# Kernel tuning notes

Hardware: AMD Instinct MI355X
Metric: run time of the kernel (lower is better)

The kernel has to match this reference:

```python
import jax, jax.numpy as jnp
import numpy as np

B, C, L = 8, 256, 4096
OC = C // 2  # out_channels default
EPS = 1e-5


def setup_inputs() -> dict:
    key = jax.random.key(0)
    ks = jax.random.split(key, 12)
    s_in = 1.0 / np.sqrt(C)   # conv1d default init scale (kaiming-uniform-ish)
    s_oc = 1.0 / np.sqrt(OC)
    return {
        "x": jax.random.normal(ks[0], (B, C, L), dtype=jnp.float32),
        "g_w": jax.random.uniform(ks[1], (OC, C), jnp.float32, -s_in, s_in),
        "g_b": jax.random.uniform(ks[2], (OC,), jnp.float32, -s_in, s_in),
        # theta/phi weights: nn.init.normal_(w, 0.02) -> mean 0.02, std 1
        "theta_w": 0.02 + jax.random.normal(ks[3], (OC, C), dtype=jnp.float32),
        "theta_b": jax.random.uniform(ks[4], (OC,), jnp.float32, -s_in, s_in),
        "phi_w": 0.02 + jax.random.normal(ks[5], (OC, C), dtype=jnp.float32),
        "phi_b": jax.random.uniform(ks[6], (OC,), jnp.float32, -s_in, s_in),
        "W_w": jax.random.uniform(ks[7], (C, OC), jnp.float32, -s_oc, s_oc),
        "W_b": jax.random.uniform(ks[8], (C,), jnp.float32, -s_oc, s_oc),
        # BN affine: init to zero in the original; use small random for a meaningful test
        "gamma": 0.1 * jax.random.normal(ks[9], (C,), dtype=jnp.float32),
        "beta": 0.1 * jax.random.normal(ks[10], (C,), dtype=jnp.float32),
    }


def reference(x, g_w, g_b, theta_w, theta_b, phi_w, phi_b, W_w, W_b, gamma, beta):
    # x: (b, c, l). 1x1 conv == per-position linear map over channels.
    g_x = jnp.einsum('oc,bcl->bol', g_w, x) + g_b[None, :, None]        # (b, oc, l)
    theta_x = jnp.einsum('oc,bcl->bol', theta_w, x) + theta_b[None, :, None]
    phi_x = jnp.einsum('oc,bcl->bol', phi_w, x) + phi_b[None, :, None]
    # f = theta^T phi : (b, l, l) quadratic score matrix (no softmax)
    f = jnp.einsum('bok,bom->bkm', theta_x, phi_x)
    N = f.shape[-1]
    # y = (f @ g^T) / N, returned in (b, oc, l) layout
    y = jnp.einsum('bkm,bom->bok', f, g_x) / N
    W_y = jnp.einsum('co,bol->bcl', W_w, y) + W_b[None, :, None]        # (b, c, l)
    # BatchNorm1d (training mode: batch statistics over (b, l), biased var)
    mean = jnp.mean(W_y, axis=(0, 2), keepdims=True)
    var = jnp.mean((W_y - mean) ** 2, axis=(0, 2), keepdims=True)
    W_y = (W_y - mean) * jax.lax.rsqrt(var + EPS)
    W_y = gamma[None, :, None] * W_y + beta[None, :, None]
    return W_y + x  # residual
```

## Files before the change

kernel.cpp:

```cpp
#include <hip/hip_runtime.h>
#include <hip/hip_bf16.h>

#define B_ 8
#define C_ 256
#define OC_ 128
#define L_ 4096
#define EPS_ 1e-5f
#define SPLITK 8

typedef unsigned short u16;
typedef __attribute__((ext_vector_type(4))) unsigned short u16x4;
typedef __attribute__((ext_vector_type(4))) float f32x4;
typedef __attribute__((ext_vector_type(8))) short bf16x8;

__device__ inline u16 f2bf(float f) {
  union { __hip_bfloat16 h; u16 u; } v;
  v.h = __float2bfloat16(f);
  return v.u;
}
__device__ inline float bf2f(u16 u) {
  union { float f; unsigned u; } v;
  v.u = ((unsigned)u) << 16;
  return v.f;
}

__device__ inline void gload_lds16(const void* g, void* lds) {
  __builtin_amdgcn_global_load_lds(
      (const __attribute__((address_space(1))) unsigned int*)g,
      (__attribute__((address_space(3))) unsigned int*)lds, 16, 0, 0);
}

__global__ __launch_bounds__(256) void k_cvt(const float* __restrict__ x,
                                             u16* __restrict__ Xb,
                                             u16* __restrict__ XbT,
                                             float* __restrict__ spartial) {
  __shared__ u16 T[64][73];
  __shared__ float P[64][17];
  const int b = blockIdx.z, c0 = blockIdx.y * 64, l0 = blockIdx.x * 64;
  const int tid = threadIdx.x;
#pragma unroll
  for (int it = 0; it < 4; ++it) {
    int idx = it * 256 + tid;
    int row = idx >> 4;
    int col = (idx & 15) << 2;
    size_t gi = ((size_t)(b * C_ + c0 + row)) * L_ + l0 + col;
    float4 v = *(const float4*)(x + gi);
    u16 u0 = f2bf(v.x), u1 = f2bf(v.y), u2 = f2bf(v.z), u3 = f2bf(v.w);
    u16x4 u = {u0, u1, u2, u3};
    *(u16x4*)(Xb + gi) = u;
    T[row][col] = u0; T[row][col + 1] = u1; T[row][col + 2] = u2; T[row][col + 3] = u3;
    P[row][idx & 15] = v.x + v.y + v.z + v.w;
  }
  __syncthreads();
  if (tid < 64) {
    float acc = 0.f;
#pragma unroll
    for (int j = 0; j < 16; j++) acc += P[tid][j];
    spartial[(size_t)blockIdx.x * (B_ * C_) + b * C_ + c0 + tid] = acc;
  }
#pragma unroll
  for (int it = 0; it < 4; ++it) {
    int idx = it * 256 + tid;
    int lrow = idx >> 4;
    int ccol = (idx & 15) << 2;
    u16x4 u = {T[ccol][lrow], T[ccol + 1][lrow], T[ccol + 2][lrow], T[ccol + 3][lrow]};
    *(u16x4*)(XbT + ((size_t)b * L_ + l0 + lrow) * C_ + c0 + ccol) = u;
  }
}

__global__ __launch_bounds__(256) void k_xxt(const u16* __restrict__ Xb,
                                             float* __restrict__ Spart) {
  const int b = blockIdx.z, split = blockIdx.y;
  const int ti = blockIdx.x >> 2, tj = blockIdx.x & 3;
  __shared__ u16 lds[2][2][64 * 64];
  const int tid = threadIdx.x, lane = tid & 63;
  const int wid = tid >> 6, wr = wid >> 1, wc = wid & 1;
  const u16* Arows = Xb + ((size_t)b * C_ + ti * 64) * L_;
  const u16* Brows = Xb + ((size_t)b * C_ + tj * 64) * L_;
  const int k0 = split * (L_ / SPLITK);
  f32x4 acc[2][2] = {};

  auto STAGE = [&](int buf, int kt) {
#pragma unroll
    for (int ch = 0; ch < 2; ch++) {
      int d = ch * 4096 + tid * 16;
      int row = d >> 7;
      int kb = (d & 127) ^ ((row & 7) << 4);
      gload_lds16(Arows + (size_t)row * L_ + k0 + kt + (kb >> 1), (char*)lds[buf][0] + d);
      gload_lds16(Brows + (size_t)row * L_ + k0 + kt + (kb >> 1), (char*)lds[buf][1] + d);
    }
  };

  STAGE(0, 0);
  asm volatile("s_waitcnt vmcnt(0)" ::: "memory");
  __syncthreads();
  int cur = 0;
  for (int kt = 0; kt < L_ / SPLITK; kt += 64) {
    if (kt + 64 < L_ / SPLITK) STAGE(cur ^ 1, kt + 64);
#pragma unroll
    for (int kk = 0; kk < 2; kk++) {
      bf16x8 af[2], bfr[2];
#pragma unroll
      for (int m = 0; m < 2; m++) {
        int row = wr * 32 + m * 16 + (lane & 15);
        int kb = ((kk << 6) + ((lane >> 4) << 4)) ^ ((row & 7) << 4);
        af[m] = *(const bf16x8*)((const char*)lds[cur][0] + row * 128 + kb);
      }
#pragma unroll
      for (int n = 0; n < 2; n++) {
        int row = wc * 32 + n * 16 + (lane & 15);
        int kb = ((kk << 6) + ((lane >> 4) << 4)) ^ ((row & 7) << 4);
        bfr[n] = *(const bf16x8*)((const char*)lds[cur][1] + row * 128 + kb);
      }
#pragma unroll
      for (int m = 0; m < 2; m++)
#pragma unroll
        for (int n = 0; n < 2; n++)
          acc[m][n] = __builtin_amdgcn_mfma_f32_16x16x32_bf16(af[m], bfr[n], acc[m][n], 0, 0, 0);
    }
    asm volatile("s_waitcnt vmcnt(0)" ::: "memory");
    __syncthreads();
    cur ^= 1;
  }
  float* Sp = Spart + ((size_t)split * B_ + b) * C_ * C_;
#pragma unroll
  for (int m = 0; m < 2; m++)
#pragma unroll
    for (int n = 0; n < 2; n++) {
      int r0 = ti * 64 + wr * 32 + m * 16 + ((lane >> 4) << 2);
      int c0 = tj * 64 + wc * 32 + n * 16 + (lane & 15);
#pragma unroll
      for (int r = 0; r < 4; r++)
        Sp[(size_t)(r0 + r) * C_ + c0] = acc[m][n][r];
    }
}

__global__ __launch_bounds__(256) void k_sreduce(const float* __restrict__ Spart,
                                                 const float* __restrict__ spartial,
                                                 const float* __restrict__ g_w,
                                                 float* __restrict__ S,
                                                 u16* __restrict__ Sb,
                                                 float* __restrict__ s,
                                                 float* __restrict__ gwT) {
  const int bid = blockIdx.x, tid = threadIdx.x;
  if (bid < (B_ * C_ * C_) / 256) {
    size_t idx = (size_t)bid * 256 + tid;
    float acc = 0.f;
    for (int sp = 0; sp < SPLITK; sp++) acc += Spart[(size_t)sp * B_ * C_ * C_ + idx];
    S[idx] = acc;
    Sb[idx] = f2bf(acc);
  } else if (bid < (B_ * C_ * C_) / 256 + (B_ * C_) / 256) {
    int idx2 = (bid - (B_ * C_ * C_) / 256) * 256 + tid;
    float acc = 0.f;
#pragma unroll 8
    for (int i = 0; i < 64; i++) acc += spartial[(size_t)i * (B_ * C_) + idx2];
    s[idx2] = acc;
  } else {
    int t = bid - ((B_ * C_ * C_) / 256 + (B_ * C_) / 256);
    int o = t * 8 + (tid & 7);
    int cbase = (tid >> 3) * 8;
#pragma unroll
    for (int k = 0; k < 8; k++) {
      int c = cbase + k;
      gwT[c * OC_ + o] = g_w[o * C_ + c];
    }
  }
}

__global__ __launch_bounds__(256) void k_mid1(const float* __restrict__ S,
                                              const float* __restrict__ s,
                                              const float* __restrict__ phi_w,
                                              const float* __restrict__ phi_b,
                                              const float* __restrict__ gwT,
                                              const float* __restrict__ g_b,
                                              float* __restrict__ MT) {
  const int b = blockIdx.x >> 5, ot = blockIdx.x & 31;
  const int tid = threadIdx.x;
  __shared__ float pw[4][257], t2[4][257], sl[256], ps_s[4], pb_s[4], redw[4][4];
  sl[tid] = s[b * C_ + tid];
#pragma unroll
  for (int r = 0; r < 4; r++) pw[r][tid] = phi_w[(ot * 4 + r) * C_ + tid];
  if (tid < 4) pb_s[tid] = phi_b[ot * 4 + tid];
  __syncthreads();
  float acc4[4] = {};
  const float* Sbr = S + (size_t)b * C_ * C_;
#pragma unroll 4
  for (int cp = 0; cp < C_; cp++) {
    float sv = Sbr[(size_t)cp * C_ + tid];
#pragma unroll
    for (int r = 0; r < 4; r++) acc4[r] += pw[r][cp] * sv;
  }
  const int lane = tid & 63, w = tid >> 6;
#pragma unroll
  for (int r = 0; r < 4; r++) {
    float v = pw[r][tid] * sl[tid];
#pragma unroll
    for (int off = 1; off < 64; off <<= 1) v += __shfl_xor(v, off, 64);
    if (lane == 0) redw[w][r] = v;
  }
#pragma unroll
  for (int r = 0; r < 4; r++) t2[r][tid] = acc4[r] + pb_s[r] * sl[tid];
  __syncthreads();
  if (tid < 4) ps_s[tid] = redw[0][tid] + redw[1][tid] + redw[2][tid] + redw[3][tid];
  __syncthreads();
  const int o = tid & 127, half = tid >> 7;
  float m0 = 0.f, m1 = 0.f;
#pragma unroll 4
  for (int c = 0; c < C_; c++) {
    float gv = gwT[c * OC_ + o];
    m0 += t2[half * 2][c] * gv;
    m1 += t2[half * 2 + 1][c] * gv;
  }
  float gb = g_b[o];
  int r0 = half * 2;
  MT[((size_t)b * OC_ + o) * OC_ + ot * 4 + r0]     = m0 + (ps_s[r0] + (float)L_ * pb_s[r0]) * gb;
  MT[((size_t)b * OC_ + o) * OC_ + ot * 4 + r0 + 1] = m1 + (ps_s[r0 + 1] + (float)L_ * pb_s[r0 + 1]) * gb;
}

__global__ __launch_bounds__(256) void k_mid2(const float* __restrict__ MT,
                                              const float* __restrict__ W_w,
                                              const float* __restrict__ theta_w,
                                              const float* __restrict__ theta_b,
                                              const float* __restrict__ W_b,
                                              const float* __restrict__ s,
                                              u16* __restrict__ Qb,
                                              float* __restrict__ qv,
                                              float* __restrict__ qs_g,
                                              float* __restrict__ sum1) {
  const int b = blockIdx.x >> 6, ct = blockIdx.x & 63;
  const int c0 = ct * 4;
  const int tid = threadIdx.x;
  __shared__ float ww[4][OC_], u_s[4][OC_ + 2], s_l[C_], q_s[4], redq[4][4];
  s_l[tid] = s[b * C_ + tid];
#pragma unroll
  for (int i = tid; i < 4 * OC_; i += 256)
    ww[i >> 7][i & 127] = W_w[(c0 + (i >> 7)) * OC_ + (i & 127)];
  __syncthreads();
  const int op = tid & 127, rh = tid >> 7;
  float ua0 = 0.f, ua1 = 0.f;
  const float* MTb = MT + (size_t)b * OC_ * OC_;
#pragma unroll 4
  for (int o = 0; o < OC_; o++) {
    float mv = MTb[(size_t)o * OC_ + op];
    ua0 += ww[rh * 2][o] * mv;
    ua1 += ww[rh * 2 + 1][o] * mv;
  }
  u_s[rh * 2][op] = ua0 * (1.f / (float)L_);
  u_s[rh * 2 + 1][op] = ua1 * (1.f / (float)L_);
  __syncthreads();
  {
    const int r = tid >> 6, lane = tid & 63;
    float v = u_s[r][lane] * theta_b[lane] + u_s[r][lane + 64] * theta_b[lane + 64];
#pragma unroll
    for (int off = 1; off < 64; off <<= 1) v += __shfl_xor(v, off, 64);
    if (lane == 0) {
      float qval = v + W_b[c0 + r];
      q_s[r] = qval;
      qv[b * C_ + c0 + r] = qval;
    }
  }
  float qa[4] = {};
#pragma unroll 2
  for (int o = 0; o < OC_; o++) {
    float tv = theta_w[(size_t)o * C_ + tid];
#pragma unroll
    for (int r = 0; r < 4; r++) qa[r] += u_s[r][o] * tv;
  }
#pragma unroll
  for (int r = 0; r < 4; r++)
    Qb[((size_t)b * C_ + c0 + r) * C_ + tid] = f2bf(qa[r]);
  const int lane = tid & 63, w = tid >> 6;
#pragma unroll
  for (int r = 0; r < 4; r++) {
    float v = qa[r] * s_l[tid];
#pragma unroll
    for (int off = 1; off < 64; off <<= 1) v += __shfl_xor(v, off, 64);
    if (lane == 0) redq[w][r] = v;
  }
  __syncthreads();
  if (tid < 4) {
    float qs = redq[0][tid] + redq[1][tid] + redq[2][tid] + redq[3][tid];
    qs_g[b * C_ + c0 + tid] = qs;
    sum1[b * C_ + c0 + tid] = qs + (float)L_ * q_s[tid];
  }
}

__global__ __launch_bounds__(256) void k_ystat(const u16* __restrict__ Qb,
                                               const u16* __restrict__ Sb,
                                               float* __restrict__ e2part) {
  const int b = blockIdx.z;
  const int chs = blockIdx.y >> 1, ct = blockIdx.y & 1;
  const int ks = blockIdx.x;
  __shared__ u16 lds[2 * 128 * 64];
  __shared__ float e2s[128][2];
  const int tid = threadIdx.x, lane = tid & 63;
  const int wid = tid >> 6, wr = wid >> 1, wc = wid & 1;
  const u16* Abase = Qb + ((size_t)b * C_ + ct * 128) * C_;
  const u16* Bbase = Sb + ((size_t)b * C_ + chs * 128) * C_;
  const int k0 = ks * 64;
  f32x4 acc[4][4] = {};
#pragma unroll
  for (int ch = 0; ch < 4; ch++) {
    int d = ch * 4096 + tid * 16;
    int row = d >> 7;
    int kb = (d & 127) ^ ((row & 7) << 4);
    gload_lds16(Abase + (size_t)row * C_ + k0 + (kb >> 1), (char*)lds + d);
    gload_lds16(Bbase + (size_t)row * C_ + k0 + (kb >> 1), (char*)lds + 16384 + d);
  }
  asm volatile("s_waitcnt vmcnt(0)" ::: "memory");
  __syncthreads();
#pragma unroll
  for (int kk = 0; kk < 2; kk++) {
    bf16x8 af[4], bfr[4];
#pragma unroll
    for (int m = 0; m < 4; m++) {
      int row = wr * 64 + m * 16 + (lane & 15);
      int kb = ((kk << 6) + ((lane >> 4) << 4)) ^ ((row & 7) << 4);
      af[m] = *(const bf16x8*)((const char*)lds + row * 128 + kb);
    }
#pragma unroll
    for (int n = 0; n < 4; n++) {
      int row = wc * 64 + n * 16 + (lane & 15);
      int kb = ((kk << 6) + ((lane >> 4) << 4)) ^ ((row & 7) << 4);
      bfr[n] = *(const bf16x8*)((const char*)lds + 16384 + row * 128 + kb);
    }
#pragma unroll
    for (int m = 0; m < 4; m++)
#pragma unroll
      for (int n = 0; n < 4; n++)
        acc[m][n] = __builtin_amdgcn_mfma_f32_16x16x32_bf16(af[m], bfr[n], acc[m][n], 0, 0, 0);
  }
  float e2a[4][4];
#pragma unroll
  for (int m = 0; m < 4; m++)
#pragma unroll
    for (int r = 0; r < 4; r++) e2a[m][r] = 0.f;
#pragma unroll
  for (int m = 0; m < 4; m++)
#pragma unroll
    for (int n = 0; n < 4; n++) {
      int ch = chs * 128 + wc * 64 + n * 16 + (lane & 15);
#pragma unroll
      for (int r = 0; r < 4; r++) {
        int c_loc = wr * 64 + m * 16 + ((lane >> 4) << 2) + r;
        float q2 = bf2f(Qb[((size_t)b * C_ + ct * 128 + c_loc) * C_ + ch]);
        e2a[m][r] += acc[m][n][r] * q2;
      }
    }
#pragma unroll
  for (int m = 0; m < 4; m++)
#pragma unroll
    for (int r = 0; r < 4; r++) {
      float v = e2a[m][r];
      v += __shfl_xor(v, 1, 64);
      v += __shfl_xor(v, 2, 64);
      v += __shfl_xor(v, 4, 64);
      v += __shfl_xor(v, 8, 64);
      if ((lane & 15) == 0) {
        int c_loc = wr * 64 + m * 16 + ((lane >> 4) << 2) + r;
        e2s[c_loc][wc] = v;
      }
    }
  __syncthreads();
  if (tid < 128)
    e2part[(((size_t)chs * 4 + ks) * B_ + b) * C_ + ct * 128 + tid] =
        e2s[tid][0] + e2s[tid][1];
}

__global__ __launch_bounds__(256) void k_fin(const float* __restrict__ sum1,
                                             const float* __restrict__ e2part,
                                             const float* __restrict__ qv,
                                             const float* __restrict__ qs_g,
                                             const float* __restrict__ gamma,
                                             const float* __restrict__ beta,
                                             float* __restrict__ gsc_g,
                                             float* __restrict__ qp_g) {
  const int b = blockIdx.x, c = threadIdx.x;
  float m = 0.f, e = 0.f;
#pragma unroll
  for (int bb = 0; bb < B_; bb++) {
    m += sum1[bb * C_ + c];
    float e2 = 0.f;
#pragma unroll
    for (int sl = 0; sl < 8; sl++) e2 += e2part[((size_t)sl * B_ + bb) * C_ + c];
    float qq = qv[bb * C_ + c], qs = qs_g[bb * C_ + c];
    e += e2 + 2.f * qq * qs + (float)L_ * qq * qq;
  }
  const float inv_n = 1.f / (float)(B_ * L_);
  m *= inv_n;
  e *= inv_n;
  float var = e - m * m;
  float g = gamma[c] * rsqrtf(var + EPS_);
  if (b == 0) gsc_g[c] = g;
  qp_g[b * C_ + c] = g * (qv[b * C_ + c] - m) + beta[c];
}

__global__ __launch_bounds__(256) void k_out(const u16* __restrict__ Qb,
                                             const float* __restrict__ gsc_g,
                                             const float* __restrict__ qp_g,
                                             const u16* __restrict__ XbT,
                                             const u16* __restrict__ Xb,
                                             float* __restrict__ out) {
  const int b = blockIdx.z, ct = blockIdx.y, lt = blockIdx.x;
  __shared__ u16 lds[2][2 * 128 * 64];
  __shared__ float gsc_s[128], qp_s[128];
  const int tid = threadIdx.x, lane = tid & 63;
  const int wid = tid >> 6, wr = wid >> 1, wc = wid & 1;
  if (tid < 128) {
    gsc_s[tid] = gsc_g[ct * 128 + tid];
    qp_s[tid] = qp_g[b * C_ + ct * 128 + tid];
  }
  const u16* Abase = Qb + ((size_t)b * C_ + ct * 128) * C_;
  const u16* Bbase = XbT + ((size_t)b * L_ + lt * 128) * C_;
  f32x4 acc[4][4] = {};
  auto STAGE = [&](int buf, int k0) {
#pragma unroll
    for (int ch = 0; ch < 4; ch++) {
      int d = ch * 4096 + tid * 16;
      int row = d >> 7;
      int kb = (d & 127) ^ ((row & 7) << 4);
      gload_lds16(Abase + (size_t)row * C_ + k0 + (kb >> 1), (char*)lds[buf] + d);
      gload_lds16(Bbase + (size_t)row * C_ + k0 + (kb >> 1), (char*)lds[buf] + 16384 + d);
    }
  };
  STAGE(0, 0);
  asm volatile("s_waitcnt vmcnt(0)" ::: "memory");
  __syncthreads();
  int cur = 0;
  for (int k0 = 0; k0 < C_; k0 += 64) {
    if (k0 + 64 < C_) STAGE(cur ^ 1, k0 + 64);
#pragma unroll
    for (int kk = 0; kk < 2; kk++) {
      bf16x8 af[4], bfr[4];
#pragma unroll
      for (int m = 0; m < 4; m++) {
        int row = wr * 64 + m * 16 + (lane & 15);
        int kb = ((kk << 6) + ((lane >> 4) << 4)) ^ ((row & 7) << 4);
        af[m] = *(const bf16x8*)((const char*)lds[cur] + row * 128 + kb);
      }
#pragma unroll
      for (int n = 0; n < 4; n++) {
        int row = wc * 64 + n * 16 + (lane & 15);
        int kb = ((kk << 6) + ((lane >> 4) << 4)) ^ ((row & 7) << 4);
        bfr[n] = *(const bf16x8*)((const char*)lds[cur] + 16384 + row * 128 + kb);
      }
#pragma unroll
      for (int m = 0; m < 4; m++)
#pragma unroll
        for (int n = 0; n < 4; n++)
          acc[m][n] = __builtin_amdgcn_mfma_f32_16x16x32_bf16(af[m], bfr[n], acc[m][n], 0, 0, 0);
    }
    asm volatile("s_waitcnt vmcnt(0)" ::: "memory");
    __syncthreads();
    cur ^= 1;
  }
#pragma unroll
  for (int m = 0; m < 4; m++)
#pragma unroll
    for (int n = 0; n < 4; n++) {
      int cl = wr * 64 + m * 16 + ((lane >> 4) << 2);
      int c = ct * 128 + cl;
      int l = lt * 128 + wc * 64 + n * 16 + (lane & 15);
#pragma unroll
      for (int r = 0; r < 4; r++) {
        size_t gi = ((size_t)b * C_ + c + r) * L_ + l;
        out[gi] = gsc_s[cl + r] * acc[m][n][r] + bf2f(Xb[gi]) + qp_s[cl + r];
      }
    }
}

extern "C" void kernel_launch(void* const* d_in, const int* in_sizes, int n_in,
                              void* d_out, int out_size, void* d_ws, size_t ws_size,
                              hipStream_t stream) {
  const float* x       = (const float*)d_in[0];
  const float* g_w     = (const float*)d_in[1];
  const float* g_b     = (const float*)d_in[2];
  const float* theta_w = (const float*)d_in[3];
  const float* theta_b = (const float*)d_in[4];
  const float* phi_w   = (const float*)d_in[5];
  const float* phi_b   = (const float*)d_in[6];
  const float* W_w     = (const float*)d_in[7];
  const float* W_b     = (const float*)d_in[8];
  const float* gamma   = (const float*)d_in[9];
  const float* beta    = (const float*)d_in[10];
  float* out = (float*)d_out;

  float* ws = (float*)d_ws;
  size_t off = 0;
  float* Spart    = ws + off; off += (size_t)SPLITK * B_ * C_ * C_;
  float* S        = ws + off; off += (size_t)B_ * C_ * C_;
  float* spartial = ws + off; off += (size_t)B_ * C_ * 64;
  float* s_       = ws + off; off += B_ * C_;
  float* gwT      = ws + off; off += C_ * OC_;
  float* MT       = ws + off; off += (size_t)B_ * OC_ * OC_;
  float* qv       = ws + off; off += B_ * C_;
  float* qs_g     = ws + off; off += B_ * C_;
  float* sum1     = ws + off; off += B_ * C_;
  float* e2part   = ws + off; off += 8 * B_ * C_;
  float* gsc_g    = ws + off; off += C_;
  float* qp_g     = ws + off; off += B_ * C_;
  u16* Sb  = (u16*)(ws + off); off += (size_t)B_ * C_ * C_ / 2;
  u16* Qb  = (u16*)(ws + off); off += (size_t)B_ * C_ * C_ / 2;
  u16* Xb  = (u16*)(ws + off); off += (size_t)B_ * C_ * L_ / 2;
  u16* XbT = (u16*)(ws + off); off += (size_t)B_ * C_ * L_ / 2;

  k_cvt<<<dim3(L_ / 64, C_ / 64, B_), 256, 0, stream>>>(x, Xb, XbT, spartial);
  k_xxt<<<dim3(16, SPLITK, B_), 256, 0, stream>>>(Xb, Spart);
  k_sreduce<<<(B_ * C_ * C_) / 256 + (B_ * C_) / 256 + 16, 256, 0, stream>>>(
      Spart, spartial, g_w, S, Sb, s_, gwT);
  k_mid1<<<B_ * 32, 256, 0, stream>>>(S, s_, phi_w, phi_b, gwT, g_b, MT);
  k_mid2<<<B_ * 64, 256, 0, stream>>>(MT, W_w, theta_w, theta_b, W_b, s_,
                                      Qb, qv, qs_g, sum1);
  k_ystat<<<dim3(4, 4, B_), 256, 0, stream>>>(Qb, Sb, e2part);
  k_fin<<<B_, 256, 0, stream>>>(sum1, e2part, qv, qs_g, gamma, beta, gsc_g, qp_g);
  k_out<<<dim3(L_ / 128, C_ / 128, B_), 256, 0, stream>>>(
      Qb, gsc_g, qp_g, XbT, Xb, out);
}
```

Baseline: 126.7 us.

## Precompose weight products, fuse mid kernels into MFMA Q generator, drop residual reload

Batch-independent weight products (W_w·g_w, theta_w^T·phi_w and the bias terms) are now computed in extra blocks of the conversion kernel. The per-batch reduction and the two mid kernels are replaced by a single MFMA-based kernel that reduces the split-K partials on the fly and builds Q. BatchNorm finalisation moves into the output kernel. The residual is folded into the GEMM by adding an identity to gsc·Q, so Xb is no longer re-read. SPLITK is halved, and the kernel count drops from eight to five, at the cost of a small 32-block Q stage and extra bf16 rounding of the residual path.

```diff
diff --git a/kernel.cpp b/kernel.cpp
--- a/kernel.cpp
+++ b/kernel.cpp
@@ -6,10 +6,12 @@
 #define OC_ 128
 #define L_ 4096
 #define EPS_ 1e-5f
-#define SPLITK 8
+#define SPLITK 4
+#define INV_L (1.0f / 4096.0f)
 
 typedef unsigned short u16;
 typedef __attribute__((ext_vector_type(4))) unsigned short u16x4;
+typedef __attribute__((ext_vector_type(8))) unsigned short u16x8;
 typedef __attribute__((ext_vector_type(4))) float f32x4;
 typedef __attribute__((ext_vector_type(8))) short bf16x8;
 
@@ -30,41 +32,114 @@
       (__attribute__((address_space(3))) unsigned int*)lds, 16, 0, 0);
 }
 
-__global__ __launch_bounds__(256) void k_cvt(const float* __restrict__ x,
-                                             u16* __restrict__ Xb,
-                                             u16* __restrict__ XbT,
-                                             float* __restrict__ spartial) {
+__global__ __launch_bounds__(256) void k_cvt(
+    const float* __restrict__ x, u16* __restrict__ Xb, u16* __restrict__ XbT,
+    float* __restrict__ spartial,
+    const float* __restrict__ W_w, const float* __restrict__ g_w,
+    const float* __restrict__ g_b, const float* __restrict__ theta_w,
+    const float* __restrict__ theta_b, const float* __restrict__ phi_w,
+    const float* __restrict__ phi_b,
+    u16* __restrict__ P1b, u16* __restrict__ P1Tb, u16* __restrict__ P2T,
+    float* __restrict__ w1, float* __restrict__ rho, float* __restrict__ p2b,
+    float* __restrict__ tbbg) {
+  const int bid = blockIdx.x, tid = threadIdx.x;
   __shared__ u16 T[64][73];
   __shared__ float P[64][17];
-  const int b = blockIdx.z, c0 = blockIdx.y * 64, l0 = blockIdx.x * 64;
-  const int tid = threadIdx.x;
-#pragma unroll
-  for (int it = 0; it < 4; ++it) {
-    int idx = it * 256 + tid;
-    int row = idx >> 4;
-    int col = (idx & 15) << 2;
-    size_t gi = ((size_t)(b * C_ + c0 + row)) * L_ + l0 + col;
-    float4 v = *(const float4*)(x + gi);
-    u16 u0 = f2bf(v.x), u1 = f2bf(v.y), u2 = f2bf(v.z), u3 = f2bf(v.w);
-    u16x4 u = {u0, u1, u2, u3};
-    *(u16x4*)(Xb + gi) = u;
-    T[row][col] = u0; T[row][col + 1] = u1; T[row][col + 2] = u2; T[row][col + 3] = u3;
-    P[row][idx & 15] = v.x + v.y + v.z + v.w;
-  }
-  __syncthreads();
-  if (tid < 64) {
-    float acc = 0.f;
-#pragma unroll
-    for (int j = 0; j < 16; j++) acc += P[tid][j];
-    spartial[(size_t)blockIdx.x * (B_ * C_) + b * C_ + c0 + tid] = acc;
-  }
-#pragma unroll
-  for (int it = 0; it < 4; ++it) {
-    int idx = it * 256 + tid;
-    int lrow = idx >> 4;
-    int ccol = (idx & 15) << 2;
-    u16x4 u = {T[ccol][lrow], T[ccol + 1][lrow], T[ccol + 2][lrow], T[ccol + 3][lrow]};
-    *(u16x4*)(XbT + ((size_t)b * L_ + l0 + lrow) * C_ + c0 + ccol) = u;
+  __shared__ float ww[32][OC_ + 1];
+  __shared__ float gbs[OC_];
+  __shared__ float tw[OC_][33];
+  __shared__ float pbs[OC_], tbs[OC_];
+  if (bid < 2048) {
+    const int b = bid >> 8, ct = (bid >> 6) & 3, lt = bid & 63;
+    const int c0 = ct * 64, l0 = lt * 64;
+#pragma unroll
+    for (int it = 0; it < 4; ++it) {
+      int idx = it * 256 + tid;
+      int row = idx >> 4;
+      int col = (idx & 15) << 2;
+      size_t gi = ((size_t)(b * C_ + c0 + row)) * L_ + l0 + col;
+      float4 v = *(const float4*)(x + gi);
+      u16 u0 = f2bf(v.x), u1_ = f2bf(v.y), u2 = f2bf(v.z), u3 = f2bf(v.w);
+      u16x4 u = {u0, u1_, u2, u3};
+      *(u16x4*)(Xb + gi) = u;
+      T[row][col] = u0; T[row][col + 1] = u1_; T[row][col + 2] = u2; T[row][col + 3] = u3;
+      P[row][idx & 15] = v.x + v.y + v.z + v.w;
+    }
+    __syncthreads();
+    if (tid < 64) {
+      float acc = 0.f;
+#pragma unroll
+      for (int j = 0; j < 16; j++) acc += P[tid][j];
+      spartial[(size_t)lt * (B_ * C_) + b * C_ + c0 + tid] = acc;
+    }
+#pragma unroll
+    for (int it = 0; it < 4; ++it) {
+      int idx = it * 256 + tid;
+      int lrow = idx >> 4;
+      int ccol = (idx & 15) << 2;
+      u16x4 u = {T[ccol][lrow], T[ccol + 1][lrow], T[ccol + 2][lrow], T[ccol + 3][lrow]};
+      *(u16x4*)(XbT + ((size_t)b * L_ + l0 + lrow) * C_ + c0 + ccol) = u;
+    }
+  } else if (bid < 2056) {
+    const int cbase = (bid - 2048) * 32;
+    for (int i = tid; i < 32 * OC_; i += 256)
+      ww[i >> 7][i & 127] = W_w[(size_t)(cbase + (i >> 7)) * OC_ + (i & 127)];
+    if (tid < OC_) gbs[tid] = g_b[tid];
+    __syncthreads();
+    float acc[32] = {};
+    for (int o = 0; o < OC_; o++) {
+      float gv = g_w[(size_t)o * C_ + tid];
+#pragma unroll
+      for (int r = 0; r < 32; r++) acc[r] += ww[r][o] * gv;
+    }
+    u16 tr[32];
+#pragma unroll
+    for (int r = 0; r < 32; r++) {
+      u16 h = f2bf(acc[r]);
+      P1b[(size_t)(cbase + r) * C_ + tid] = h;
+      tr[r] = h;
+    }
+#pragma unroll
+    for (int k = 0; k < 4; k++) {
+      u16x8 v;
+#pragma unroll
+      for (int j = 0; j < 8; j++) v[j] = tr[k * 8 + j];
+      *(u16x8*)(P1Tb + (size_t)tid * C_ + cbase + k * 8) = v;
+    }
+    if (tid < 32) {
+      float a = 0.f;
+      for (int o = 0; o < OC_; o++) a += ww[tid][o] * gbs[o];
+      w1[cbase + tid] = a;
+    }
+  } else {
+    const int c2base = (bid - 2056) * 32;
+    for (int i = tid; i < OC_ * 32; i += 256) {
+      int op = i >> 5, r = i & 31;
+      tw[op][r] = theta_w[(size_t)op * C_ + c2base + r];
+    }
+    if (tid < OC_) { pbs[tid] = phi_b[tid]; tbs[tid] = theta_b[tid]; }
+    __syncthreads();
+    float acc[32] = {};
+    float ap2b = 0.f;
+    for (int op = 0; op < OC_; op++) {
+      float pv = phi_w[(size_t)op * C_ + tid];
+#pragma unroll
+      for (int r = 0; r < 32; r++) acc[r] += tw[op][r] * pv;
+      ap2b += tbs[op] * pv;
+    }
+#pragma unroll
+    for (int r = 0; r < 32; r++) P2T[(size_t)(c2base + r) * C_ + tid] = f2bf(acc[r]);
+    if (bid == 2056) p2b[tid] = ap2b;
+    if (tid < 32) {
+      float a = 0.f;
+      for (int op = 0; op < OC_; op++) a += pbs[op] * tw[op][tid];
+      rho[c2base + tid] = a;
+    }
+    if (bid == 2056 && tid == 0) {
+      float a = 0.f;
+      for (int op = 0; op < OC_; op++) a += pbs[op] * tbs[op];
+      tbbg[0] = a;
+    }
   }
 }
 
@@ -135,158 +210,197 @@
     }
 }
 
-__global__ __launch_bounds__(256) void k_sreduce(const float* __restrict__ Spart,
-                                                 const float* __restrict__ spartial,
-                                                 const float* __restrict__ g_w,
-                                                 float* __restrict__ S,
-                                                 u16* __restrict__ Sb,
-                                                 float* __restrict__ s,
-                                                 float* __restrict__ gwT) {
-  const int bid = blockIdx.x, tid = threadIdx.x;
-  if (bid < (B_ * C_ * C_) / 256) {
-    size_t idx = (size_t)bid * 256 + tid;
-    float acc = 0.f;
-    for (int sp = 0; sp < SPLITK; sp++) acc += Spart[(size_t)sp * B_ * C_ * C_ + idx];
-    S[idx] = acc;
-    Sb[idx] = f2bf(acc);
-  } else if (bid < (B_ * C_ * C_) / 256 + (B_ * C_) / 256) {
-    int idx2 = (bid - (B_ * C_ * C_) / 256) * 256 + tid;
-    float acc = 0.f;
-#pragma unroll 8
-    for (int i = 0; i < 64; i++) acc += spartial[(size_t)i * (B_ * C_) + idx2];
-    s[idx2] = acc;
-  } else {
-    int t = bid - ((B_ * C_ * C_) / 256 + (B_ * C_) / 256);
-    int o = t * 8 + (tid & 7);
-    int cbase = (tid >> 3) * 8;
-#pragma unroll
-    for (int k = 0; k < 8; k++) {
-      int c = cbase + k;
-      gwT[c * OC_ + o] = g_w[o * C_ + c];
-    }
-  }
-}
-
-__global__ __launch_bounds__(256) void k_mid1(const float* __restrict__ S,
-                                              const float* __restrict__ s,
-                                              const float* __restrict__ phi_w,
-                                              const float* __restrict__ phi_b,
-                                              const float* __restrict__ gwT,
-                                              const float* __restrict__ g_b,
-                                              float* __restrict__ MT) {
-  const int b = blockIdx.x >> 5, ot = blockIdx.x & 31;
-  const int tid = threadIdx.x;
-  __shared__ float pw[4][257], t2[4][257], sl[256], ps_s[4], pb_s[4], redw[4][4];
-  sl[tid] = s[b * C_ + tid];
-#pragma unroll
-  for (int r = 0; r < 4; r++) pw[r][tid] = phi_w[(ot * 4 + r) * C_ + tid];
-  if (tid < 4) pb_s[tid] = phi_b[ot * 4 + tid];
+__global__ __launch_bounds__(256) void k_qgen(
+    const float* __restrict__ Spart, const float* __restrict__ spartial,
+    const u16* __restrict__ P1b, const u16* __restrict__ P1Tb,
+    const u16* __restrict__ P2T,
+    const float* __restrict__ w1g, const float* __restrict__ rho,
+    const float* __restrict__ p2b, const float* __restrict__ tbbg,
+    const float* __restrict__ W_b,
+    u16* __restrict__ Qb, float* __restrict__ qv, float* __restrict__ qspart) {
+  const int js = blockIdx.x, b = blockIdx.y;
+  const int tid = threadIdx.x, lane = tid & 63, wid = tid >> 6;
+  __shared__ u16 Abuf[256 * 64];
+  __shared__ u16 Bbuf[64 * 64];
+  __shared__ u16 Tt[64][264];
+  __shared__ float s_l[C_], u1_l[C_], z_l[C_], p2b_l[C_], w1_l[C_];
+  __shared__ float v1_l[64], red[4];
+  {
+    float a = 0.f;
+    for (int lt = 0; lt < 64; lt++) a += spartial[(size_t)lt * (B_ * C_) + b * C_ + tid];
+    s_l[tid] = a;
+    p2b_l[tid] = p2b[tid];
+    w1_l[tid] = w1g[tid];
+  }
+  float part = s_l[tid] * p2b_l[tid];
+#pragma unroll
+  for (int off = 1; off < 64; off <<= 1) part += __shfl_xor(part, off, 64);
+  if (lane == 0) red[wid] = part;
   __syncthreads();
-  float acc4[4] = {};
-  const float* Sbr = S + (size_t)b * C_ * C_;
+  const float sp2b = red[0] + red[1] + red[2] + red[3];
+  f32x4 acc[4][4] = {};
+  for (int kt = 0; kt < C_; kt += 64) {
+    __syncthreads();
+    {
+      const int jr = (tid & 15) * 4;
+      const int rb = tid >> 4;
 #pragma unroll 4
-  for (int cp = 0; cp < C_; cp++) {
-    float sv = Sbr[(size_t)cp * C_ + tid];
-#pragma unroll
-    for (int r = 0; r < 4; r++) acc4[r] += pw[r][cp] * sv;
-  }
-  const int lane = tid & 63, w = tid >> 6;
-#pragma unroll
-  for (int r = 0; r < 4; r++) {
-    float v = pw[r][tid] * sl[tid];
-#pragma unroll
-    for (int off = 1; off < 64; off <<= 1) v += __shfl_xor(v, off, 64);
-    if (lane == 0) redw[w][r] = v;
-  }
-#pragma unroll
-  for (int r = 0; r < 4; r++) t2[r][tid] = acc4[r] + pb_s[r] * sl[tid];
+      for (int pass = 0; pass < 16; pass++) {
+        int row = pass * 16 + rb;
+        float4 a0 = {0.f, 0.f, 0.f, 0.f};
+#pragma unroll
+        for (int sp = 0; sp < SPLITK; sp++) {
+          float4 v = *(const float4*)(Spart + ((size_t)sp * B_ + b) * (C_ * C_) +
+                                      (size_t)row * C_ + kt + jr);
+          a0.x += v.x; a0.y += v.y; a0.z += v.z; a0.w += v.w;
+        }
+        u16x4 h = {f2bf(a0.x), f2bf(a0.y), f2bf(a0.z), f2bf(a0.w)};
+        int byte = (jr * 2) ^ ((row & 7) << 4);
+        *(u16x4*)((char*)Abuf + row * 128 + byte) = h;
+      }
+#pragma unroll
+      for (int ch = 0; ch < 2; ch++) {
+        int d = ch * 4096 + tid * 16;
+        int row = d >> 7;
+        int kb = (d & 127) ^ ((row & 7) << 4);
+        gload_lds16(P2T + (size_t)(js * 64 + row) * C_ + kt + (kb >> 1), (char*)Bbuf + d);
+      }
+    }
+    asm volatile("s_waitcnt vmcnt(0)" ::: "memory");
+    __syncthreads();
+#pragma unroll
+    for (int kk = 0; kk < 2; kk++) {
+      bf16x8 af[4], bfr[4];
+#pragma unroll
+      for (int m = 0; m < 4; m++) {
+        int row = wid * 64 + m * 16 + (lane & 15);
+        int kb = ((kk << 6) + ((lane >> 4) << 4)) ^ ((row & 7) << 4);
+        af[m] = *(const bf16x8*)((const char*)Abuf + row * 128 + kb);
+      }
+#pragma unroll
+      for (int n = 0; n < 4; n++) {
+        int row = n * 16 + (lane & 15);
+        int kb = ((kk << 6) + ((lane >> 4) << 4)) ^ ((row & 7) << 4);
+        bfr[n] = *(const bf16x8*)((const char*)Bbuf + row * 128 + kb);
+      }
+#pragma unroll
+      for (int m = 0; m < 4; m++)
+#pragma unroll
+        for (int n = 0; n < 4; n++)
+          acc[m][n] = __builtin_amdgcn_mfma_f32_16x16x32_bf16(af[m], bfr[n], acc[m][n], 0, 0, 0);
+    }
+  }
+#pragma unroll
+  for (int m = 0; m < 4; m++)
+#pragma unroll
+    for (int n = 0; n < 4; n++) {
+      int j = n * 16 + (lane & 15);
+      int t0 = wid * 64 + m * 16 + ((lane >> 4) << 2);
+      u16x4 h = {f2bf(acc[m][n][0]), f2bf(acc[m][n][1]), f2bf(acc[m][n][2]), f2bf(acc[m][n][3])};
+      *(u16x4*)((char*)&Tt[0][0] + j * 528 + t0 * 2) = h;
+    }
+  {
+    float a = 0.f;
+    for (int cp = 0; cp < C_; cp++) a += bf2f(P1Tb[(size_t)cp * C_ + tid]) * s_l[cp];
+    u1_l[tid] = a;
+  }
+  if (tid < 64) {
+    float a = 0.f;
+    const u16x8* pr = (const u16x8*)(P2T + (size_t)(js * 64 + tid) * C_);
+    for (int i = 0; i < 32; i++) {
+      u16x8 v = pr[i];
+#pragma unroll
+      for (int k = 0; k < 8; k++) a += bf2f(v[k]) * s_l[i * 8 + k];
+    }
+    v1_l[tid] = a;
+  }
+  if (js == 0) {
+    float a = 0.f;
+    for (int sp = 0; sp < SPLITK; sp++)
+      for (int cp = 0; cp < C_; cp++)
+        a += Spart[((size_t)sp * B_ + b) * (C_ * C_) + (size_t)cp * C_ + tid] * p2b_l[cp];
+    z_l[tid] = a;
+  }
   __syncthreads();
-  if (tid < 4) ps_s[tid] = redw[0][tid] + redw[1][tid] + redw[2][tid] + redw[3][tid];
-  __syncthreads();
-  const int o = tid & 127, half = tid >> 7;
-  float m0 = 0.f, m1 = 0.f;
-#pragma unroll 4
-  for (int c = 0; c < C_; c++) {
-    float gv = gwT[c * OC_ + o];
-    m0 += t2[half * 2][c] * gv;
-    m1 += t2[half * 2 + 1][c] * gv;
-  }
-  float gb = g_b[o];
-  int r0 = half * 2;
-  MT[((size_t)b * OC_ + o) * OC_ + ot * 4 + r0]     = m0 + (ps_s[r0] + (float)L_ * pb_s[r0]) * gb;
-  MT[((size_t)b * OC_ + o) * OC_ + ot * 4 + r0 + 1] = m1 + (ps_s[r0 + 1] + (float)L_ * pb_s[r0 + 1]) * gb;
-}
-
-__global__ __launch_bounds__(256) void k_mid2(const float* __restrict__ MT,
-                                              const float* __restrict__ W_w,
-                                              const float* __restrict__ theta_w,
-                                              const float* __restrict__ theta_b,
-                                              const float* __restrict__ W_b,
-                                              const float* __restrict__ s,
-                                              u16* __restrict__ Qb,
-                                              float* __restrict__ qv,
-                                              float* __restrict__ qs_g,
-                                              float* __restrict__ sum1) {
-  const int b = blockIdx.x >> 6, ct = blockIdx.x & 63;
-  const int c0 = ct * 4;
-  const int tid = threadIdx.x;
-  __shared__ float ww[4][OC_], u_s[4][OC_ + 2], s_l[C_], q_s[4], redq[4][4];
-  s_l[tid] = s[b * C_ + tid];
-#pragma unroll
-  for (int i = tid; i < 4 * OC_; i += 256)
-    ww[i >> 7][i & 127] = W_w[(c0 + (i >> 7)) * OC_ + (i & 127)];
-  __syncthreads();
-  const int op = tid & 127, rh = tid >> 7;
-  float ua0 = 0.f, ua1 = 0.f;
-  const float* MTb = MT + (size_t)b * OC_ * OC_;
-#pragma unroll 4
-  for (int o = 0; o < OC_; o++) {
-    float mv = MTb[(size_t)o * OC_ + op];
-    ua0 += ww[rh * 2][o] * mv;
-    ua1 += ww[rh * 2 + 1][o] * mv;
-  }
-  u_s[rh * 2][op] = ua0 * (1.f / (float)L_);
-  u_s[rh * 2 + 1][op] = ua1 * (1.f / (float)L_);
-  __syncthreads();
-  {
-    const int r = tid >> 6, lane = tid & 63;
-    float v = u_s[r][lane] * theta_b[lane] + u_s[r][lane + 64] * theta_b[lane + 64];
-#pragma unroll
-    for (int off = 1; off < 64; off <<= 1) v += __shfl_xor(v, off, 64);
-    if (lane == 0) {
-      float qval = v + W_b[c0 + r];
-      q_s[r] = qval;
-      qv[b * C_ + c0 + r] = qval;
-    }
-  }
-  float qa[4] = {};
-#pragma unroll 2
-  for (int o = 0; o < OC_; o++) {
-    float tv = theta_w[(size_t)o * C_ + tid];
-#pragma unroll
-    for (int r = 0; r < 4; r++) qa[r] += u_s[r][o] * tv;
-  }
-#pragma unroll
-  for (int r = 0; r < 4; r++)
-    Qb[((size_t)b * C_ + c0 + r) * C_ + tid] = f2bf(qa[r]);
-  const int lane = tid & 63, w = tid >> 6;
-#pragma unroll
-  for (int r = 0; r < 4; r++) {
-    float v = qa[r] * s_l[tid];
-#pragma unroll
-    for (int off = 1; off < 64; off <<= 1) v += __shfl_xor(v, off, 64);
-    if (lane == 0) redq[w][r] = v;
-  }
-  __syncthreads();
-  if (tid < 4) {
-    float qs = redq[0][tid] + redq[1][tid] + redq[2][tid] + redq[3][tid];
-    qs_g[b * C_ + c0 + tid] = qs;
-    sum1[b * C_ + c0 + tid] = qs + (float)L_ * q_s[tid];
+  if (js == 0) {
+    float qq = 0.f;
+    for (int cp = 0; cp < C_; cp++) qq += bf2f(P1Tb[(size_t)cp * C_ + tid]) * z_l[cp];
+    float tbb = tbbg[0];
+    float w1c = w1_l[tid];
+    qv[b * C_ + tid] = INV_L * (qq + w1c * sp2b + u1_l[tid] * tbb) + w1c * tbb + W_b[tid];
+  }
+  f32x4 acc2[4][4] = {};
+  for (int kt = 0; kt < C_; kt += 64) {
+    __syncthreads();
+#pragma unroll
+    for (int ch = 0; ch < 8; ch++) {
+      int d = ch * 4096 + tid * 16;
+      int row = d >> 7;
+      int kb = (d & 127) ^ ((row & 7) << 4);
+      gload_lds16(P1b + (size_t)row * C_ + kt + (kb >> 1), (char*)Abuf + d);
+    }
+    asm volatile("s_waitcnt vmcnt(0)" ::: "memory");
+    __syncthreads();
+#pragma unroll
+    for (int kk = 0; kk < 2; kk++) {
+      bf16x8 af[4], bfr[4];
+#pragma unroll
+      for (int m = 0; m < 4; m++) {
+        int row = wid * 64 + m * 16 + (lane & 15);
+        int kb = ((kk << 6) + ((lane >> 4) << 4)) ^ ((row & 7) << 4);
+        af[m] = *(const bf16x8*)((const char*)Abuf + row * 128 + kb);
+      }
+#pragma unroll
+      for (int n = 0; n < 4; n++) {
+        int j = n * 16 + (lane & 15);
+        int ke = kt + kk * 32 + ((lane >> 4) << 3);
+        bfr[n] = *(const bf16x8*)((const char*)&Tt[0][0] + j * 528 + ke * 2);
+      }
+#pragma unroll
+      for (int m = 0; m < 4; m++)
+#pragma unroll
+        for (int n = 0; n < 4; n++)
+          acc2[m][n] = __builtin_amdgcn_mfma_f32_16x16x32_bf16(af[m], bfr[n], acc2[m][n], 0, 0, 0);
+    }
+  }
+  float rho_j[4], v1_j[4];
+#pragma unroll
+  for (int n = 0; n < 4; n++) {
+    rho_j[n] = rho[js * 64 + n * 16 + (lane & 15)];
+    v1_j[n] = v1_l[n * 16 + (lane & 15)];
+  }
+#pragma unroll
+  for (int m = 0; m < 4; m++) {
+    int c0 = wid * 64 + m * 16 + ((lane >> 4) << 2);
+    float qsp_acc[4] = {};
+#pragma unroll
+    for (int n = 0; n < 4; n++) {
+      int jg = js * 64 + n * 16 + (lane & 15);
+      float sj = s_l[jg];
+#pragma unroll
+      for (int r = 0; r < 4; r++) {
+        int c = c0 + r;
+        float q = INV_L * acc2[m][n][r] + w1_l[c] * (INV_L * v1_j[n] + rho_j[n]) +
+                  INV_L * u1_l[c] * rho_j[n];
+        Qb[((size_t)b * C_ + c) * C_ + jg] = f2bf(q);
+        qsp_acc[r] += q * sj;
+      }
+    }
+#pragma unroll
+    for (int r = 0; r < 4; r++) {
+      float v = qsp_acc[r];
+      v += __shfl_xor(v, 1, 64);
+      v += __shfl_xor(v, 2, 64);
+      v += __shfl_xor(v, 4, 64);
+      v += __shfl_xor(v, 8, 64);
+      if ((lane & 15) == 0)
+        qspart[((size_t)js * B_ + b) * C_ + c0 + r] = v;
+    }
   }
 }
 
 __global__ __launch_bounds__(256) void k_ystat(const u16* __restrict__ Qb,
-                                               const u16* __restrict__ Sb,
+                                               const float* __restrict__ Spart,
                                                float* __restrict__ e2part) {
   const int b = blockIdx.z;
   const int chs = blockIdx.y >> 1, ct = blockIdx.y & 1;
@@ -296,7 +410,6 @@
   const int tid = threadIdx.x, lane = tid & 63;
   const int wid = tid >> 6, wr = wid >> 1, wc = wid & 1;
   const u16* Abase = Qb + ((size_t)b * C_ + ct * 128) * C_;
-  const u16* Bbase = Sb + ((size_t)b * C_ + chs * 128) * C_;
   const int k0 = ks * 64;
   f32x4 acc[4][4] = {};
 #pragma unroll
@@ -305,7 +418,24 @@
     int row = d >> 7;
     int kb = (d & 127) ^ ((row & 7) << 4);
     gload_lds16(Abase + (size_t)row * C_ + k0 + (kb >> 1), (char*)lds + d);
-    gload_lds16(Bbase + (size_t)row * C_ + k0 + (kb >> 1), (char*)lds + 16384 + d);
+  }
+  {
+    const int jr = (tid & 15) * 4;
+    const int rb = tid >> 4;
+#pragma unroll 4
+    for (int pass = 0; pass < 8; pass++) {
+      int row = pass * 16 + rb;
+      float4 a0 = {0.f, 0.f, 0.f, 0.f};
+#pragma unroll
+      for (int sp = 0; sp < SPLITK; sp++) {
+        float4 v = *(const float4*)(Spart + ((size_t)sp * B_ + b) * (C_ * C_) +
+                                    (size_t)(chs * 128 + row) * C_ + k0 + jr);
+        a0.x += v.x; a0.y += v.y; a0.z += v.z; a0.w += v.w;
+      }
+      u16x4 h = {f2bf(a0.x), f2bf(a0.y), f2bf(a0.z), f2bf(a0.w)};
+      int byte = (jr * 2) ^ ((row & 7) << 4);
+      *(u16x4*)((char*)lds + 16384 + row * 128 + byte) = h;
+    }
   }
   asm volatile("s_waitcnt vmcnt(0)" ::: "memory");
   __syncthreads();
@@ -367,68 +497,94 @@
         e2s[tid][0] + e2s[tid][1];
 }
 
-__global__ __launch_bounds__(256) void k_fin(const float* __restrict__ sum1,
+__global__ __launch_bounds__(256) void k_out(const u16* __restrict__ Qb,
+                                             const float* __restrict__ qv,
+                                             const float* __restrict__ qspart,
                                              const float* __restrict__ e2part,
-                                             const float* __restrict__ qv,
-                                             const float* __restrict__ qs_g,
                                              const float* __restrict__ gamma,
                                              const float* __restrict__ beta,
-                                             float* __restrict__ gsc_g,
-                                             float* __restrict__ qp_g) {
-  const int b = blockIdx.x, c = threadIdx.x;
-  float m = 0.f, e = 0.f;
-#pragma unroll
-  for (int bb = 0; bb < B_; bb++) {
-    m += sum1[bb * C_ + c];
-    float e2 = 0.f;
-#pragma unroll
-    for (int sl = 0; sl < 8; sl++) e2 += e2part[((size_t)sl * B_ + bb) * C_ + c];
-    float qq = qv[bb * C_ + c], qs = qs_g[bb * C_ + c];
-    e += e2 + 2.f * qq * qs + (float)L_ * qq * qq;
-  }
-  const float inv_n = 1.f / (float)(B_ * L_);
-  m *= inv_n;
-  e *= inv_n;
-  float var = e - m * m;
-  float g = gamma[c] * rsqrtf(var + EPS_);
-  if (b == 0) gsc_g[c] = g;
-  qp_g[b * C_ + c] = g * (qv[b * C_ + c] - m) + beta[c];
-}
-
-__global__ __launch_bounds__(256) void k_out(const u16* __restrict__ Qb,
-                                             const float* __restrict__ gsc_g,
-                                             const float* __restrict__ qp_g,
                                              const u16* __restrict__ XbT,
-                                             const u16* __restrict__ Xb,
                                              float* __restrict__ out) {
   const int b = blockIdx.z, ct = blockIdx.y, lt = blockIdx.x;
-  __shared__ u16 lds[2][2 * 128 * 64];
+  __shared__ u16 Albs[2][128 * 64];
+  __shared__ u16 Blbs[2][128 * 64];
   __shared__ float gsc_s[128], qp_s[128];
   const int tid = threadIdx.x, lane = tid & 63;
   const int wid = tid >> 6, wr = wid >> 1, wc = wid & 1;
   if (tid < 128) {
-    gsc_s[tid] = gsc_g[ct * 128 + tid];
-    qp_s[tid] = qp_g[b * C_ + ct * 128 + tid];
-  }
-  const u16* Abase = Qb + ((size_t)b * C_ + ct * 128) * C_;
+    int c = ct * 128 + tid;
+    float m_ = 0.f, e_ = 0.f;
+#pragma unroll
+    for (int bb = 0; bb < B_; bb++) {
+      float qsv = 0.f;
+#pragma unroll
+      for (int jss = 0; jss < 4; jss++) qsv += qspart[((size_t)jss * B_ + bb) * C_ + c];
+      float qvv = qv[bb * C_ + c];
+      m_ += qsv + (float)L_ * qvv;
+      float e2 = 0.f;
+#pragma unroll
+      for (int sl = 0; sl < 8; sl++) e2 += e2part[((size_t)sl * B_ + bb) * C_ + c];
+      e_ += e2 + 2.f * qvv * qsv + (float)L_ * qvv * qvv;
+    }
+    const float inv_n = 1.f / (float)(B_ * L_);
+    m_ *= inv_n;
+    e_ *= inv_n;
+    float var = e_ - m_ * m_;
+    float g = gamma[c] * rsqrtf(var + EPS_);
+    gsc_s[tid] = g;
+    qp_s[tid] = g * (qv[b * C_ + c] - m_) + beta[c];
+  }
+  __syncthreads();
   const u16* Bbase = XbT + ((size_t)b * L_ + lt * 128) * C_;
   f32x4 acc[4][4] = {};
-  auto STAGE = [&](int buf, int k0) {
+  u16x4 regs[8];
+  const int jr = (tid & 15) * 4;
+  const int rb = tid >> 4;
+  auto LOADA = [&](int k0) {
+#pragma unroll
+    for (int pass = 0; pass < 8; pass++) {
+      int row = pass * 16 + rb;
+      regs[pass] = *(const u16x4*)(Qb + ((size_t)b * C_ + ct * 128 + row) * C_ + k0 + jr);
+    }
+  };
+  auto WRITEA = [&](int buf, int k0) {
+#pragma unroll
+    for (int pass = 0; pass < 8; pass++) {
+      int row = pass * 16 + rb;
+      float g = gsc_s[row];
+      int c = ct * 128 + row;
+      u16x4 h;
+#pragma unroll
+      for (int i = 0; i < 4; i++) {
+        float a = g * bf2f(regs[pass][i]);
+        if (k0 + jr + i == c) a += 1.f;
+        h[i] = f2bf(a);
+      }
+      int byte = (jr * 2) ^ ((row & 7) << 4);
+      *(u16x4*)((char*)Albs[buf] + row * 128 + byte) = h;
+    }
+  };
+  auto STAGEB = [&](int buf, int k0) {
 #pragma unroll
     for (int ch = 0; ch < 4; ch++) {
       int d = ch * 4096 + tid * 16;
       int row = d >> 7;
       int kb = (d & 127) ^ ((row & 7) << 4);
-      gload_lds16(Abase + (size_t)row * C_ + k0 + (kb >> 1), (char*)lds[buf] + d);
-      gload_lds16(Bbase + (size_t)row * C_ + k0 + (kb >> 1), (char*)lds[buf] + 16384 + d);
+      gload_lds16(Bbase + (size_t)row * C_ + k0 + (kb >> 1), (char*)Blbs[buf] + d);
     }
   };
-  STAGE(0, 0);
+  LOADA(0);
+  STAGEB(0, 0);
   asm volatile("s_waitcnt vmcnt(0)" ::: "memory");
+  WRITEA(0, 0);
   __syncthreads();
   int cur = 0;
   for (int k0 = 0; k0 < C_; k0 += 64) {
-    if (k0 + 64 < C_) STAGE(cur ^ 1, k0 + 64);
+    bool hasNext = (k0 + 64 < C_);
+    if (hasNext) {
+      STAGEB(cur ^ 1, k0 + 64);
+      LOADA(k0 + 64);
+    }
 #pragma unroll
     for (int kk = 0; kk < 2; kk++) {
       bf16x8 af[4], bfr[4];
@@ -436,13 +592,13 @@
       for (int m = 0; m < 4; m++) {
         int row = wr * 64 + m * 16 + (lane & 15);
         int kb = ((kk << 6) + ((lane >> 4) << 4)) ^ ((row & 7) << 4);
-        af[m] = *(const bf16x8*)((const char*)lds[cur] + row * 128 + kb);
+        af[m] = *(const bf16x8*)((const char*)Albs[cur] + (row & 127) * 128 + kb);
       }
 #pragma unroll
       for (int n = 0; n < 4; n++) {
         int row = wc * 64 + n * 16 + (lane & 15);
         int kb = ((kk << 6) + ((lane >> 4) << 4)) ^ ((row & 7) << 4);
-        bfr[n] = *(const bf16x8*)((const char*)lds[cur] + 16384 + row * 128 + kb);
+        bfr[n] = *(const bf16x8*)((const char*)Blbs[cur] + row * 128 + kb);
       }
 #pragma unroll
       for (int m = 0; m < 4; m++)
@@ -450,7 +606,10 @@
         for (int n = 0; n < 4; n++)
           acc[m][n] = __builtin_amdgcn_mfma_f32_16x16x32_bf16(af[m], bfr[n], acc[m][n], 0, 0, 0);
     }
-    asm volatile("s_waitcnt vmcnt(0)" ::: "memory");
+    if (hasNext) {
+      asm volatile("s_waitcnt vmcnt(0)" ::: "memory");
+      WRITEA(cur ^ 1, k0 + 64);
+    }
     __syncthreads();
     cur ^= 1;
   }
@@ -464,7 +623,7 @@
 #pragma unroll
       for (int r = 0; r < 4; r++) {
         size_t gi = ((size_t)b * C_ + c + r) * L_ + l;
-        out[gi] = gsc_s[cl + r] * acc[m][n][r] + bf2f(Xb[gi]) + qp_s[cl + r];
+        out[gi] = acc[m][n][r] + qp_s[cl + r];
       }
     }
 }
@@ -488,31 +647,28 @@
   float* ws = (float*)d_ws;
   size_t off = 0;
   float* Spart    = ws + off; off += (size_t)SPLITK * B_ * C_ * C_;
-  float* S        = ws + off; off += (size_t)B_ * C_ * C_;
   float* spartial = ws + off; off += (size_t)B_ * C_ * 64;
-  float* s_       = ws + off; off += B_ * C_;
-  float* gwT      = ws + off; off += C_ * OC_;
-  float* MT       = ws + off; off += (size_t)B_ * OC_ * OC_;
   float* qv       = ws + off; off += B_ * C_;
-  float* qs_g     = ws + off; off += B_ * C_;
-  float* sum1     = ws + off; off += B_ * C_;
+  float* qspart   = ws + off; off += 4 * B_ * C_;
   float* e2part   = ws + off; off += 8 * B_ * C_;
-  float* gsc_g    = ws + off; off += C_;
-  float* qp_g     = ws + off; off += B_ * C_;
-  u16* Sb  = (u16*)(ws + off); off += (size_t)B_ * C_ * C_ / 2;
-  u16* Qb  = (u16*)(ws + off); off += (size_t)B_ * C_ * C_ / 2;
-  u16* Xb  = (u16*)(ws + off); off += (size_t)B_ * C_ * L_ / 2;
-  u16* XbT = (u16*)(ws + off); off += (size_t)B_ * C_ * L_ / 2;
-
-  k_cvt<<<dim3(L_ / 64, C_ / 64, B_), 256, 0, stream>>>(x, Xb, XbT, spartial);
+  float* w1       = ws + off; off += C_;
+  float* rho      = ws + off; off += C_;
+  float* p2b      = ws + off; off += C_;
+  float* tbbg     = ws + off; off += 64;
+  u16* P1b  = (u16*)(ws + off); off += C_ * C_ / 2;
+  u16* P1Tb = (u16*)(ws + off); off += C_ * C_ / 2;
+  u16* P2T  = (u16*)(ws + off); off += C_ * C_ / 2;
+  u16* Qb   = (u16*)(ws + off); off += (size_t)B_ * C_ * C_ / 2;
+  u16* Xb   = (u16*)(ws + off); off += (size_t)B_ * C_ * L_ / 2;
+  u16* XbT  = (u16*)(ws + off); off += (size_t)B_ * C_ * L_ / 2;
+
+  k_cvt<<<2064, 256, 0, stream>>>(x, Xb, XbT, spartial, W_w, g_w, g_b, theta_w,
+                                  theta_b, phi_w, phi_b, P1b, P1Tb, P2T, w1, rho,
+                                  p2b, tbbg);
   k_xxt<<<dim3(16, SPLITK, B_), 256, 0, stream>>>(Xb, Spart);
-  k_sreduce<<<(B_ * C_ * C_) / 256 + (B_ * C_) / 256 + 16, 256, 0, stream>>>(
-      Spart, spartial, g_w, S, Sb, s_, gwT);
-  k_mid1<<<B_ * 32, 256, 0, stream>>>(S, s_, phi_w, phi_b, gwT, g_b, MT);
-  k_mid2<<<B_ * 64, 256, 0, stream>>>(MT, W_w, theta_w, theta_b, W_b, s_,
-                                      Qb, qv, qs_g, sum1);
-  k_ystat<<<dim3(4, 4, B_), 256, 0, stream>>>(Qb, Sb, e2part);
-  k_fin<<<B_, 256, 0, stream>>>(sum1, e2part, qv, qs_g, gamma, beta, gsc_g, qp_g);
+  k_qgen<<<dim3(4, B_), 256, 0, stream>>>(Spart, spartial, P1b, P1Tb, P2T, w1,
+                                          rho, p2b, tbbg, W_b, Qb, qv, qspart);
+  k_ystat<<<dim3(4, 4, B_), 256, 0, stream>>>(Qb, Spart, e2part);
   k_out<<<dim3(L_ / 128, C_ / 128, B_), 256, 0, stream>>>(
-      Qb, gsc_g, qp_g, XbT, Xb, out);
-}
+      Qb, qv, qspart, e2part, gamma, beta, XbT, out);
+}
```

Result: slower. 147.1 us (+16.1%).
